# Optimization experiments

Measured on AMD Instinct MI355X. Metric: run time of the kernel, lower is better.

## Reference

```python
import jax, jax.numpy as jnp
import numpy as np

H, KV, D, HID = 16, 8, 128, 2048  # n_heads, n_kv_heads, head_dim, hidden_size
EPS = 1e-6
SCALE = D ** -0.5


def rotate_half(x):
    x1, x2 = x[..., : x.shape[-1] // 2], x[..., x.shape[-1] // 2 :]
    return jnp.concatenate((-x2, x1), axis=-1)


def rms_norm(x, w, eps=EPS):
    xf = x.astype(jnp.float32)
    xf = xf * jax.lax.rsqrt(jnp.mean(jnp.square(xf), axis=-1, keepdims=True) + eps)
    return (w * xf).astype(x.dtype)


def setup_inputs() -> dict:
    key = jax.random.key(0)
    ks = jax.random.split(key, 8)
    B, S = 2, 2048
    x = jax.random.normal(ks[0], (B, S, HID), dtype=jnp.float32)
    # RoPE tables from rope_theta frequencies
    theta = 5e6
    inv_freq = 1.0 / (theta ** (np.arange(0, D, 2, dtype=np.float32) / D))  # (D/2,)
    pos = np.arange(S, dtype=np.float32)
    freqs = np.outer(pos, inv_freq)  # (S, D/2)
    emb = np.concatenate([freqs, freqs], axis=-1)  # (S, D)
    sin = jnp.broadcast_to(jnp.asarray(np.sin(emb)), (B, S, D)).astype(jnp.float32)
    cos = jnp.broadcast_to(jnp.asarray(np.cos(emb)), (B, S, D)).astype(jnp.float32)
    # causal additive mask (B, 1, S, S)
    causal = jnp.where(jnp.tril(jnp.ones((S, S), dtype=bool)), 0.0, -1e9).astype(jnp.float32)
    attention_mask = jnp.broadcast_to(causal[None, None], (B, 1, S, S))
    std = 0.02
    Wq = jax.random.normal(ks[1], (HID, H * D), dtype=jnp.float32) * std
    Wk = jax.random.normal(ks[2], (HID, KV * D), dtype=jnp.float32) * std
    Wv = jax.random.normal(ks[3], (HID, KV * D), dtype=jnp.float32) * std
    Wo = jax.random.normal(ks[4], (H * D, HID), dtype=jnp.float32) * std
    q_norm_w = jnp.ones((D,), dtype=jnp.float32)
    k_norm_w = jnp.ones((D,), dtype=jnp.float32)
    return dict(x=x, sin=sin, cos=cos, attention_mask=attention_mask,
                Wq=Wq, Wk=Wk, Wv=Wv, Wo=Wo, q_norm_w=q_norm_w, k_norm_w=k_norm_w)


def reference(x, sin, cos, attention_mask, Wq, Wk, Wv, Wo, q_norm_w, k_norm_w):
    B, S, _ = x.shape
    groups = H // KV
    q = (x @ Wq).reshape(B, S, H, D)
    k = (x @ Wk).reshape(B, S, KV, D)
    v = (x @ Wv).reshape(B, S, KV, D)
    q = rms_norm(q, q_norm_w)
    k = rms_norm(k, k_norm_w)
    c, s = cos[:, :, None, :], sin[:, :, None, :]
    q = q * c + rotate_half(q) * s
    k = k * c + rotate_half(k) * s
    if groups > 1:
        k = jnp.repeat(k, groups, axis=2)  # (B,S,H,D)
        v = jnp.repeat(v, groups, axis=2)
    attn = jnp.einsum('bihd,bjhd->bhij', q, k) * SCALE  # (B,H,S,S)
    attn = jax.nn.softmax(attn + attention_mask, axis=-1)
    out = jnp.einsum('bhij,bjhd->bihd', attn, v).reshape(B, S, H * D)
    return out @ Wo
```

## Files before the change

kernel.cpp:

```cpp
#include <hip/hip_runtime.h>
#include <hip/hip_bf16.h>
#include <math.h>

#define H_    16
#define KV_   8
#define D_    128
#define HID_  2048
#define NQKV_ 4096
#define SCALE_ 0.08838834764831845f

typedef __attribute__((ext_vector_type(8))) short bf16x8;
typedef __attribute__((ext_vector_type(4))) float f32x4;
typedef __attribute__((ext_vector_type(4))) short short4v;

__device__ inline unsigned short f2bf(float f) {
  unsigned u = __builtin_bit_cast(unsigned, f);
  u += 0x7FFF + ((u >> 16) & 1);
  return (unsigned short)(u >> 16);
}

#define GLDS16(g, l)                                                     \
  __builtin_amdgcn_global_load_lds(                                      \
      (const __attribute__((address_space(1))) void*)(g),                \
      (__attribute__((address_space(3))) void*)(l), 16, 0, 0)

__global__ __launch_bounds__(256) void f32_to_bf16(
    const float* __restrict__ in, unsigned short* __restrict__ out, int n8) {
  int i = blockIdx.x * 256 + threadIdx.x;
  if (i >= n8) return;
  const float4* p = (const float4*)in + (size_t)i * 2;
  float4 a = p[0], b = p[1];
  unsigned short o[8] = {f2bf(a.x), f2bf(a.y), f2bf(a.z), f2bf(a.w),
                         f2bf(b.x), f2bf(b.y), f2bf(b.z), f2bf(b.w)};
  *(bf16x8*)(out + (size_t)i * 8) = *(bf16x8*)o;
}

__global__ __launch_bounds__(256) void transpose_bf16(
    const float* __restrict__ in, unsigned short* __restrict__ out, int K, int N) {
  __shared__ float t[32][33];
  const int k0 = blockIdx.y * 32, n0 = blockIdx.x * 32;
  const int r = threadIdx.x >> 3, c4 = (threadIdx.x & 7) * 4;
  float4 v = *(const float4*)(in + (size_t)(k0 + r) * N + n0 + c4);
  t[r][c4 + 0] = v.x; t[r][c4 + 1] = v.y; t[r][c4 + 2] = v.z; t[r][c4 + 3] = v.w;
  __syncthreads();
  unsigned short o[4];
#pragma unroll
  for (int j = 0; j < 4; ++j) o[j] = f2bf(t[c4 + j][r]);
  *(short4v*)(out + (size_t)(n0 + r) * K + k0 + c4) = *(short4v*)o;
}

#define TBM 128
#define TBN 128
#define TBK 64

template <int EPI>
__global__ __launch_bounds__(256) void gemm_bf16(
    const unsigned short* __restrict__ A,
    const unsigned short* __restrict__ Bt,
    float* __restrict__ C0, float* __restrict__ C1,
    unsigned short* __restrict__ C2, int M, int N, int K, int S) {
  __shared__ unsigned short As[TBM * TBK];
  __shared__ unsigned short Bs[TBN * TBK];
  const int tid = threadIdx.x;
  const int w = tid >> 6, lane = tid & 63;
  const int wm = w >> 1, wn = w & 1;
  const int fr = lane & 15, fq = lane >> 4;
  const int row0 = blockIdx.y * TBM, col0 = blockIdx.x * TBN;

  const unsigned short* Ab = A + (size_t)row0 * K;
  const unsigned short* Bb = Bt + (size_t)col0 * K;
  const int sm = lane >> 3;
  const int sk = (lane & 7) * 8;

  f32x4 acc[4][4] = {};

  for (int k0 = 0; k0 < K; k0 += TBK) {
    __syncthreads();
#pragma unroll
    for (int p = 0; p < 4; ++p) {
      const int seg = w * 4 + p;
      const int m = seg * 8 + sm;
      GLDS16(Ab + (size_t)m * K + k0 + sk, As + seg * 512);
      GLDS16(Bb + (size_t)m * K + k0 + sk, Bs + seg * 512);
    }
    __syncthreads();
#pragma unroll
    for (int s = 0; s < 2; ++s) {
      bf16x8 af[4], bfr[4];
#pragma unroll
      for (int i = 0; i < 4; ++i)
        af[i] = *(const bf16x8*)(As + (wm * 64 + i * 16 + fr) * TBK + s * 32 + fq * 8);
#pragma unroll
      for (int j = 0; j < 4; ++j)
        bfr[j] = *(const bf16x8*)(Bs + (wn * 64 + j * 16 + fr) * TBK + s * 32 + fq * 8);
#pragma unroll
      for (int i = 0; i < 4; ++i)
#pragma unroll
        for (int j = 0; j < 4; ++j)
          acc[i][j] = __builtin_amdgcn_mfma_f32_16x16x32_bf16(af[i], bfr[j], acc[i][j], 0, 0, 0);
    }
  }

  if constexpr (EPI == 0) {
#pragma unroll
    for (int i = 0; i < 4; ++i)
#pragma unroll
      for (int j = 0; j < 4; ++j) {
        const int col = col0 + wn * 64 + j * 16 + fr;
#pragma unroll
        for (int r = 0; r < 4; ++r) {
          const int row = row0 + wm * 64 + i * 16 + fq * 4 + r;
          C0[(size_t)row * N + col] = acc[i][j][r];
        }
      }
  } else {
    if (col0 < H_ * D_) {
#pragma unroll
      for (int i = 0; i < 4; ++i)
#pragma unroll
        for (int j = 0; j < 4; ++j) {
          const int col = col0 + wn * 64 + j * 16 + fr;
#pragma unroll
          for (int r = 0; r < 4; ++r) {
            const int row = row0 + wm * 64 + i * 16 + fq * 4 + r;
            C0[(size_t)row * (H_ * D_) + col] = acc[i][j][r];
          }
        }
    } else if (col0 < H_ * D_ + KV_ * D_) {
#pragma unroll
      for (int i = 0; i < 4; ++i)
#pragma unroll
        for (int j = 0; j < 4; ++j) {
          const int col = col0 - H_ * D_ + wn * 64 + j * 16 + fr;
#pragma unroll
          for (int r = 0; r < 4; ++r) {
            const int row = row0 + wm * 64 + i * 16 + fq * 4 + r;
            C1[(size_t)row * (KV_ * D_) + col] = acc[i][j][r];
          }
        }
    } else {
#pragma unroll
      for (int i = 0; i < 4; ++i)
#pragma unroll
        for (int j = 0; j < 4; ++j) {
          const int cc = col0 - (H_ * D_ + KV_ * D_) + wn * 64 + j * 16 + fr;
          const int kvh = cc >> 7, d = cc & 127;
          const int row = row0 + wm * 64 + i * 16 + fq * 4;
          const int b = row / S, s = row - b * S;
          unsigned short o[4] = {f2bf(acc[i][j][0]), f2bf(acc[i][j][1]),
                                 f2bf(acc[i][j][2]), f2bf(acc[i][j][3])};
          *(short4v*)(C2 + ((size_t)(b * KV_ + kvh) * D_ + d) * S + s) = *(short4v*)o;
        }
    }
  }
}

__global__ __launch_bounds__(256) void rmsnorm_rope_o16(
    const float* __restrict__ p, unsigned short* __restrict__ o16,
    const float* __restrict__ w, const float* __restrict__ cs,
    const float* __restrict__ sn, int nheads) {
  const int row  = blockIdx.x * 4 + (threadIdx.x >> 6);
  const int lane = threadIdx.x & 63;
  const float* base = p + (size_t)row * D_;
  float x1 = base[lane];
  float x2 = base[lane + 64];
  float ss = x1 * x1 + x2 * x2;
#pragma unroll
  for (int m = 32; m; m >>= 1) ss += __shfl_xor(ss, m);
  float r = rsqrtf(ss * (1.0f / 128.0f) + 1e-6f);
  const size_t sidx = (size_t)(row / nheads) * D_;
  float n1 = x1 * r * w[lane];
  float n2 = x2 * r * w[lane + 64];
  unsigned short* ob = o16 + (size_t)row * D_;
  ob[lane]      = f2bf(n1 * cs[sidx + lane]      - n2 * sn[sidx + lane]);
  ob[lane + 64] = f2bf(n2 * cs[sidx + lane + 64] + n1 * sn[sidx + lane + 64]);
}

__global__ __launch_bounds__(256) void flash_bf16(
    const unsigned short* __restrict__ Qb, const unsigned short* __restrict__ Kb,
    const unsigned short* __restrict__ Vt, unsigned short* __restrict__ O,
    int S, int nqt) {
  __shared__ unsigned short Kt[64 * 128];
  __shared__ unsigned short Vs[128 * 64];
  __shared__ unsigned short Pl[4][16 * 64];
  const int h = blockIdx.y, b = blockIdx.z;
  const int kvh = h >> 1;
  const int tid = threadIdx.x, w = tid >> 6, lane = tid & 63;
  const int fr = lane & 15, fq = lane >> 4;
  const unsigned short* vhead = Vt + (size_t)(b * KV_ + kvh) * D_ * S;

#pragma unroll 1
  for (int half = 0; half < 2; ++half) {
    const int qt = half ? (nqt - 1 - (int)blockIdx.x) : (int)blockIdx.x;
    const int q0 = qt * 64;

    bf16x8 qf[4];
    {
      const unsigned short* qp =
          Qb + ((size_t)(b * S + q0 + w * 16 + fr) * H_ + h) * D_;
#pragma unroll
      for (int s = 0; s < 4; ++s) qf[s] = *(const bf16x8*)(qp + s * 32 + fq * 8);
    }

    f32x4 acco[8] = {};
    float mrow[4] = {-1e30f, -1e30f, -1e30f, -1e30f};
    float lrow[4] = {0.f, 0.f, 0.f, 0.f};

    for (int kt = 0; kt <= qt; ++kt) {
      __syncthreads();
#pragma unroll
      for (int p = 0; p < 4; ++p) {
        const int seg = w * 4 + p;
        {
          const int kv = seg * 4 + (lane >> 4);
          const int ch = lane & 15;
          const int gch = (ch & 8) | ((ch ^ kv) & 7);
          GLDS16(Kb + ((size_t)(b * S + kt * 64 + kv) * KV_ + kvh) * D_ + gch * 8,
                 Kt + seg * 512);
        }
        {
          const int d = seg * 8 + (lane >> 3);
          const int c = lane & 7;
          const int gc = c ^ (d & 7);
          GLDS16(vhead + (size_t)d * S + kt * 64 + gc * 8, Vs + seg * 512);
        }
      }
      __syncthreads();

      f32x4 sa[4];
      __builtin_amdgcn_s_setprio(1);
#pragma unroll
      for (int t = 0; t < 4; ++t) {
        f32x4 a = {};
        const int kv = 16 * t + fr;
#pragma unroll
        for (int s = 0; s < 4; ++s) {
          const int ch = 4 * s + fq;
          const int chs = (ch & 8) | ((ch ^ kv) & 7);
          bf16x8 kf = *(const bf16x8*)(Kt + kv * 128 + chs * 8);
          a = __builtin_amdgcn_mfma_f32_16x16x32_bf16(qf[s], kf, a, 0, 0, 0);
        }
        sa[t] = a;
      }
      __builtin_amdgcn_s_setprio(0);

#pragma unroll
      for (int t = 0; t < 4; ++t)
#pragma unroll
        for (int r = 0; r < 4; ++r) sa[t][r] *= SCALE_;
      if (kt == qt) {
#pragma unroll
        for (int t = 0; t < 4; ++t) {
          const int kvl = 16 * t + fr;
#pragma unroll
          for (int r = 0; r < 4; ++r)
            if (kvl > w * 16 + fq * 4 + r) sa[t][r] = -1e30f;
        }
      }

      float al[4];
#pragma unroll
      for (int r = 0; r < 4; ++r) {
        float mx = fmaxf(fmaxf(sa[0][r], sa[1][r]), fmaxf(sa[2][r], sa[3][r]));
        mx = fmaxf(mx, __shfl_xor(mx, 1));
        mx = fmaxf(mx, __shfl_xor(mx, 2));
        mx = fmaxf(mx, __shfl_xor(mx, 4));
        mx = fmaxf(mx, __shfl_xor(mx, 8));
        const float mn = fmaxf(mrow[r], mx);
        al[r] = __expf(mrow[r] - mn);
        mrow[r] = mn;
        float sum = 0.f;
#pragma unroll
        for (int t = 0; t < 4; ++t) {
          const float pv = __expf(sa[t][r] - mn);
          sa[t][r] = pv;
          sum += pv;
        }
        sum += __shfl_xor(sum, 1);
        sum += __shfl_xor(sum, 2);
        sum += __shfl_xor(sum, 4);
        sum += __shfl_xor(sum, 8);
        lrow[r] = lrow[r] * al[r] + sum;
#pragma unroll
        for (int c = 0; c < 8; ++c) acco[c][r] *= al[r];
      }

      unsigned short* pw = &Pl[w][0];
#pragma unroll
      for (int t = 0; t < 4; ++t) {
        const int kv = 16 * t + fr;
        const int ch = kv >> 3;
#pragma unroll
        for (int r = 0; r < 4; ++r) {
          const int q = fq * 4 + r;
          pw[q * 64 + ((ch ^ q) & 7) * 8 + (kv & 7)] = f2bf(sa[t][r]);
        }
      }

      bf16x8 pf[2];
#pragma unroll
      for (int s = 0; s < 2; ++s)
        pf[s] = *(const bf16x8*)(pw + fr * 64 + (((4 * s + fq) ^ fr) & 7) * 8);
      __builtin_amdgcn_s_setprio(1);
#pragma unroll
      for (int c = 0; c < 8; ++c) {
        const int d = 16 * c + fr;
#pragma unroll
        for (int s = 0; s < 2; ++s) {
          bf16x8 vf = *(const bf16x8*)(Vs + d * 64 + (((4 * s + fq) ^ d) & 7) * 8);
          acco[c] = __builtin_amdgcn_mfma_f32_16x16x32_bf16(pf[s], vf, acco[c], 0, 0, 0);
        }
      }
      __builtin_amdgcn_s_setprio(0);
    }

    float inv[4];
#pragma unroll
    for (int r = 0; r < 4; ++r) inv[r] = 1.0f / lrow[r];
#pragma unroll
    for (int c = 0; c < 8; ++c) {
#pragma unroll
      for (int r = 0; r < 4; ++r) {
        const int q = q0 + w * 16 + fq * 4 + r;
        O[(size_t)(b * S + q) * (H_ * D_) + h * D_ + 16 * c + fr] =
            f2bf(acco[c][r] * inv[r]);
      }
    }
  }
}

extern "C" void kernel_launch(void* const* d_in, const int* in_sizes, int n_in,
                              void* d_out, int out_size, void* d_ws, size_t ws_size,
                              hipStream_t stream) {
  const float* x  = (const float*)d_in[0];
  const float* sn = (const float*)d_in[1];
  const float* cs = (const float*)d_in[2];
  const float* Wq = (const float*)d_in[4];
  const float* Wk = (const float*)d_in[5];
  const float* Wv = (const float*)d_in[6];
  const float* Wo = (const float*)d_in[7];
  const float* qw = (const float*)d_in[8];
  const float* kw = (const float*)d_in[9];
  float* out = (float*)d_out;

  const int BS = in_sizes[0] / HID_;
  const int S  = in_sizes[3] / BS;
  const int B  = BS / S;

  float* kbuf = (float*)d_ws;
  unsigned short* vt   = (unsigned short*)(kbuf + (size_t)BS * KV_ * D_);
  unsigned short* xb   = vt + (size_t)BS * KV_ * D_;
  unsigned short* wT   = xb + (size_t)BS * HID_;
  unsigned short* qb   = wT + (size_t)NQKV_ * HID_;
  unsigned short* kb16 = qb + (size_t)BS * H_ * D_;
  unsigned short* ab16 = xb;

  dim3 blk(256);
  const int n8x = BS * HID_ / 8;

  f32_to_bf16<<<dim3(n8x / 256), blk, 0, stream>>>(x, xb, n8x);

  transpose_bf16<<<dim3((H_ * D_) / 32, HID_ / 32), blk, 0, stream>>>(Wq, wT, HID_, H_ * D_);
  transpose_bf16<<<dim3((KV_ * D_) / 32, HID_ / 32), blk, 0, stream>>>(
      Wk, wT + (size_t)(H_ * D_) * HID_, HID_, KV_ * D_);
  transpose_bf16<<<dim3((KV_ * D_) / 32, HID_ / 32), blk, 0, stream>>>(
      Wv, wT + (size_t)(H_ * D_ + KV_ * D_) * HID_, HID_, KV_ * D_);

  gemm_bf16<1><<<dim3(NQKV_ / TBN, BS / TBM), blk, 0, stream>>>(
      xb, wT, out, kbuf, vt, BS, NQKV_, HID_, S);

  rmsnorm_rope_o16<<<dim3(BS * H_ / 4),  blk, 0, stream>>>(out,  qb,   qw, cs, sn, H_);
  rmsnorm_rope_o16<<<dim3(BS * KV_ / 4), blk, 0, stream>>>(kbuf, kb16, kw, cs, sn, KV_);

  flash_bf16<<<dim3(S / 128, H_, B), blk, 0, stream>>>(qb, kb16, vt, ab16, S, S / 64);

  transpose_bf16<<<dim3(HID_ / 32, (H_ * D_) / 32), blk, 0, stream>>>(Wo, wT, H_ * D_, HID_);
  gemm_bf16<0><<<dim3(HID_ / TBN, BS / TBM), blk, 0, stream>>>(
      ab16, wT, out, nullptr, nullptr, BS, HID_, HID_, S);
}
```

Measured before the change: 426.1 us.

## Widen flash KV tile to 128, fold softmax scale into Q, merge QKV transposes

```diff
diff --git a/kernel.cpp b/kernel.cpp
--- a/kernel.cpp
+++ b/kernel.cpp
@@ -47,6 +47,26 @@
 #pragma unroll
   for (int j = 0; j < 4; ++j) o[j] = f2bf(t[c4 + j][r]);
   *(short4v*)(out + (size_t)(n0 + r) * K + k0 + c4) = *(short4v*)o;
+}
+
+__global__ __launch_bounds__(256) void transpose_qkv3(
+    const float* __restrict__ Wq, const float* __restrict__ Wk,
+    const float* __restrict__ Wv, unsigned short* __restrict__ out) {
+  __shared__ float t[32][33];
+  const int n0 = blockIdx.x * 32;
+  const int k0 = blockIdx.y * 32;
+  const float* src; int N, nloc;
+  if (n0 < H_ * D_)                  { src = Wq; N = H_ * D_;  nloc = n0; }
+  else if (n0 < H_ * D_ + KV_ * D_)  { src = Wk; N = KV_ * D_; nloc = n0 - H_ * D_; }
+  else                               { src = Wv; N = KV_ * D_; nloc = n0 - H_ * D_ - KV_ * D_; }
+  const int r = threadIdx.x >> 3, c4 = (threadIdx.x & 7) * 4;
+  float4 v = *(const float4*)(src + (size_t)(k0 + r) * N + nloc + c4);
+  t[r][c4 + 0] = v.x; t[r][c4 + 1] = v.y; t[r][c4 + 2] = v.z; t[r][c4 + 3] = v.w;
+  __syncthreads();
+  unsigned short o[4];
+#pragma unroll
+  for (int j = 0; j < 4; ++j) o[j] = f2bf(t[c4 + j][r]);
+  *(short4v*)(out + (size_t)(n0 + r) * HID_ + k0 + c4) = *(short4v*)o;
 }
 
 #define TBM 128
@@ -158,7 +178,7 @@
 __global__ __launch_bounds__(256) void rmsnorm_rope_o16(
     const float* __restrict__ p, unsigned short* __restrict__ o16,
     const float* __restrict__ w, const float* __restrict__ cs,
-    const float* __restrict__ sn, int nheads) {
+    const float* __restrict__ sn, int nheads, float oscale) {
   const int row  = blockIdx.x * 4 + (threadIdx.x >> 6);
   const int lane = threadIdx.x & 63;
   const float* base = p + (size_t)row * D_;
@@ -172,27 +192,30 @@
   float n1 = x1 * r * w[lane];
   float n2 = x2 * r * w[lane + 64];
   unsigned short* ob = o16 + (size_t)row * D_;
-  ob[lane]      = f2bf(n1 * cs[sidx + lane]      - n2 * sn[sidx + lane]);
-  ob[lane + 64] = f2bf(n2 * cs[sidx + lane + 64] + n1 * sn[sidx + lane + 64]);
+  ob[lane]      = f2bf((n1 * cs[sidx + lane]      - n2 * sn[sidx + lane])      * oscale);
+  ob[lane + 64] = f2bf((n2 * cs[sidx + lane + 64] + n1 * sn[sidx + lane + 64]) * oscale);
 }
 
 __global__ __launch_bounds__(256) void flash_bf16(
     const unsigned short* __restrict__ Qb, const unsigned short* __restrict__ Kb,
     const unsigned short* __restrict__ Vt, unsigned short* __restrict__ O,
     int S, int nqt) {
-  __shared__ unsigned short Kt[64 * 128];
-  __shared__ unsigned short Vs[128 * 64];
-  __shared__ unsigned short Pl[4][16 * 64];
+  __shared__ unsigned short Kt[128 * 128];
+  __shared__ unsigned short Vs[128 * 128];
+  __shared__ unsigned short Pl[4][16 * 128];
   const int h = blockIdx.y, b = blockIdx.z;
   const int kvh = h >> 1;
   const int tid = threadIdx.x, w = tid >> 6, lane = tid & 63;
   const int fr = lane & 15, fq = lane >> 4;
+  const int rl = lane >> 4;
+  const int sch = lane & 15;
   const unsigned short* vhead = Vt + (size_t)(b * KV_ + kvh) * D_ * S;
 
 #pragma unroll 1
   for (int half = 0; half < 2; ++half) {
     const int qt = half ? (nqt - 1 - (int)blockIdx.x) : (int)blockIdx.x;
     const int q0 = qt * 64;
+    const int nkt = (q0 + 64 + 127) >> 7;
 
     bf16x8 qf[4];
     {
@@ -206,31 +229,24 @@
     float mrow[4] = {-1e30f, -1e30f, -1e30f, -1e30f};
     float lrow[4] = {0.f, 0.f, 0.f, 0.f};
 
-    for (int kt = 0; kt <= qt; ++kt) {
+#pragma unroll 1
+    for (int kt = 0; kt < nkt; ++kt) {
       __syncthreads();
 #pragma unroll
-      for (int p = 0; p < 4; ++p) {
-        const int seg = w * 4 + p;
-        {
-          const int kv = seg * 4 + (lane >> 4);
-          const int ch = lane & 15;
-          const int gch = (ch & 8) | ((ch ^ kv) & 7);
-          GLDS16(Kb + ((size_t)(b * S + kt * 64 + kv) * KV_ + kvh) * D_ + gch * 8,
-                 Kt + seg * 512);
-        }
-        {
-          const int d = seg * 8 + (lane >> 3);
-          const int c = lane & 7;
-          const int gc = c ^ (d & 7);
-          GLDS16(vhead + (size_t)d * S + kt * 64 + gc * 8, Vs + seg * 512);
-        }
+      for (int p = 0; p < 8; ++p) {
+        const int r = p * 16 + w * 4 + rl;
+        const int gch = (sch & 8) | ((sch ^ r) & 7);
+        GLDS16(Kb + ((size_t)(b * S + kt * 128 + r) * KV_ + kvh) * D_ + gch * 8,
+               Kt + (p * 16 + w * 4) * 128);
+        GLDS16(vhead + (size_t)r * S + kt * 128 + gch * 8,
+               Vs + (p * 16 + w * 4) * 128);
       }
       __syncthreads();
 
-      f32x4 sa[4];
+      f32x4 sa[8];
       __builtin_amdgcn_s_setprio(1);
 #pragma unroll
-      for (int t = 0; t < 4; ++t) {
+      for (int t = 0; t < 8; ++t) {
         f32x4 a = {};
         const int kv = 16 * t + fr;
 #pragma unroll
@@ -244,24 +260,22 @@
       }
       __builtin_amdgcn_s_setprio(0);
 
-#pragma unroll
-      for (int t = 0; t < 4; ++t)
-#pragma unroll
-        for (int r = 0; r < 4; ++r) sa[t][r] *= SCALE_;
-      if (kt == qt) {
-#pragma unroll
-        for (int t = 0; t < 4; ++t) {
-          const int kvl = 16 * t + fr;
+      if (kt == nkt - 1) {
+#pragma unroll
+        for (int t = 0; t < 8; ++t) {
+          const int kvg = kt * 128 + 16 * t + fr;
 #pragma unroll
           for (int r = 0; r < 4; ++r)
-            if (kvl > w * 16 + fq * 4 + r) sa[t][r] = -1e30f;
+            if (kvg > q0 + w * 16 + fq * 4 + r) sa[t][r] = -1e30f;
         }
       }
 
       float al[4];
 #pragma unroll
       for (int r = 0; r < 4; ++r) {
-        float mx = fmaxf(fmaxf(sa[0][r], sa[1][r]), fmaxf(sa[2][r], sa[3][r]));
+        float mx = sa[0][r];
+#pragma unroll
+        for (int t = 1; t < 8; ++t) mx = fmaxf(mx, sa[t][r]);
         mx = fmaxf(mx, __shfl_xor(mx, 1));
         mx = fmaxf(mx, __shfl_xor(mx, 2));
         mx = fmaxf(mx, __shfl_xor(mx, 4));
@@ -271,7 +285,7 @@
         mrow[r] = mn;
         float sum = 0.f;
 #pragma unroll
-        for (int t = 0; t < 4; ++t) {
+        for (int t = 0; t < 8; ++t) {
           const float pv = __expf(sa[t][r] - mn);
           sa[t][r] = pv;
           sum += pv;
@@ -287,27 +301,30 @@
 
       unsigned short* pw = &Pl[w][0];
 #pragma unroll
-      for (int t = 0; t < 4; ++t) {
+      for (int t = 0; t < 8; ++t) {
         const int kv = 16 * t + fr;
         const int ch = kv >> 3;
 #pragma unroll
         for (int r = 0; r < 4; ++r) {
           const int q = fq * 4 + r;
-          pw[q * 64 + ((ch ^ q) & 7) * 8 + (kv & 7)] = f2bf(sa[t][r]);
-        }
-      }
-
-      bf16x8 pf[2];
-#pragma unroll
-      for (int s = 0; s < 2; ++s)
-        pf[s] = *(const bf16x8*)(pw + fr * 64 + (((4 * s + fq) ^ fr) & 7) * 8);
+          pw[q * 128 + ((ch & 8) | ((ch ^ q) & 7)) * 8 + (kv & 7)] = f2bf(sa[t][r]);
+        }
+      }
+
+      bf16x8 pf[4];
+#pragma unroll
+      for (int s = 0; s < 4; ++s) {
+        const int ch = 4 * s + fq;
+        pf[s] = *(const bf16x8*)(pw + fr * 128 + ((ch & 8) | ((ch ^ fr) & 7)) * 8);
+      }
       __builtin_amdgcn_s_setprio(1);
 #pragma unroll
       for (int c = 0; c < 8; ++c) {
         const int d = 16 * c + fr;
 #pragma unroll
-        for (int s = 0; s < 2; ++s) {
-          bf16x8 vf = *(const bf16x8*)(Vs + d * 64 + (((4 * s + fq) ^ d) & 7) * 8);
+        for (int s = 0; s < 4; ++s) {
+          const int ch = 4 * s + fq;
+          bf16x8 vf = *(const bf16x8*)(Vs + d * 128 + ((ch & 8) | ((ch ^ d) & 7)) * 8);
           acco[c] = __builtin_amdgcn_mfma_f32_16x16x32_bf16(pf[s], vf, acco[c], 0, 0, 0);
         }
       }
@@ -360,17 +377,13 @@
 
   f32_to_bf16<<<dim3(n8x / 256), blk, 0, stream>>>(x, xb, n8x);
 
-  transpose_bf16<<<dim3((H_ * D_) / 32, HID_ / 32), blk, 0, stream>>>(Wq, wT, HID_, H_ * D_);
-  transpose_bf16<<<dim3((KV_ * D_) / 32, HID_ / 32), blk, 0, stream>>>(
-      Wk, wT + (size_t)(H_ * D_) * HID_, HID_, KV_ * D_);
-  transpose_bf16<<<dim3((KV_ * D_) / 32, HID_ / 32), blk, 0, stream>>>(
-      Wv, wT + (size_t)(H_ * D_ + KV_ * D_) * HID_, HID_, KV_ * D_);
+  transpose_qkv3<<<dim3(NQKV_ / 32, HID_ / 32), blk, 0, stream>>>(Wq, Wk, Wv, wT);
 
   gemm_bf16<1><<<dim3(NQKV_ / TBN, BS / TBM), blk, 0, stream>>>(
       xb, wT, out, kbuf, vt, BS, NQKV_, HID_, S);
 
-  rmsnorm_rope_o16<<<dim3(BS * H_ / 4),  blk, 0, stream>>>(out,  qb,   qw, cs, sn, H_);
-  rmsnorm_rope_o16<<<dim3(BS * KV_ / 4), blk, 0, stream>>>(kbuf, kb16, kw, cs, sn, KV_);
+  rmsnorm_rope_o16<<<dim3(BS * H_ / 4),  blk, 0, stream>>>(out,  qb,   qw, cs, sn, H_,  SCALE_);
+  rmsnorm_rope_o16<<<dim3(BS * KV_ / 4), blk, 0, stream>>>(kbuf, kb16, kw, cs, sn, KV_, 1.0f);
 
   flash_bf16<<<dim3(S / 128, H_, B), blk, 0, stream>>>(qb, kb16, vt, ab16, S, S / 64);
 
```

Result: faster. 403.8 us (-5.2%).
